# Optimization experiments

Measured on AMD Instinct MI355X. Metric: run time of the kernel, lower is better.

The kernel has to match this reference:

```python
import jax, jax.numpy as jnp
import numpy as np

LAGS = 2
SLOPE = 0.01  # nn.LeakyReLU default negative_slope


def setup_inputs() -> dict:
    key = jax.random.key(0)
    k0, k1, k2, k3, k4 = jax.random.split(key, 5)
    B, T, D, H = 64, 514, 32, 128
    IN = LAGS * D + 1
    x = jax.random.normal(k0, (B, T, D), dtype=jnp.float32)
    # per-latent-dim 2-layer MLP params (num_layers=3, layer_norm=False collapses to 2 Linears)
    W1 = jax.random.normal(k1, (D, H, IN), dtype=jnp.float32) / np.sqrt(IN).astype(np.float32)
    b1 = jax.random.normal(k2, (D, H), dtype=jnp.float32) * 0.01
    W2 = jax.random.normal(k3, (D, H), dtype=jnp.float32) / np.sqrt(H).astype(np.float32)
    b2 = jax.random.normal(k4, (D,), dtype=jnp.float32) * 0.01
    return {"x": x, "W1": W1, "b1": b1, "W2": W2, "b2": b2}


def reference(x, W1, b1, W2, b2):
    L = LAGS
    B, T, D = x.shape
    # unfold(dim=1, size=L+1, step=1) + swapaxes -> windows [B, T-L, L+1, D]
    idx = jnp.arange(T - L)[:, None] + jnp.arange(L + 1)[None, :]
    w = x[:, idx]                       # [B, T-L, L+1, D]
    w = w.reshape(-1, L + 1, D)         # [N, L+1, D]
    yy = w[:, -1, :]                    # [N, D]  current step, per dim
    xx = w[:, :-1, :].reshape(-1, L * D)  # [N, L*D] lagged history (shared)
    # batched tiny-MLP forward: input to g_i is [xx, yy[:, i]]
    pre = (jnp.einsum('nk,dhk->ndh', xx, W1[:, :, :-1])
           + yy[:, :, None] * W1[:, :, -1][None]
           + b1[None])                  # [N, D, H]
    act = jnp.where(pre >= 0, pre, SLOPE * pre)
    residuals = jnp.einsum('ndh,dh->nd', act, W2) + b2[None]  # [N, D]
    # analytic Jacobian of scalar output wrt the (L*D+1)-dim input:
    # J = (W2 * leaky'(pre)) @ W1
    dact = jnp.where(pre >= 0, jnp.float32(1.0), jnp.float32(SLOPE))
    g = dact * W2[None]                 # [N, D, H]
    jac = jnp.einsum('ndh,dhk->ndk', g, W1)  # [N, D, L*D+1]
    logabsdet = jnp.sum(jnp.log(jnp.abs(jac[:, :, -1])), axis=1)  # [N] summed over dims
    # hist_jac: torch returns a list of D tensors [N, 1, L*D]; stacked here as [D, N, 1, L*D]
    hist_jac = jnp.transpose(jac[:, :, :-1], (1, 0, 2))[:, :, None, :]
    residuals = residuals.reshape(B, T - L, D)
    sum_log_abs_det_jacobian = logabsdet.reshape(B, T - L).sum(axis=1)  # [B]
    return residuals, sum_log_abs_det_jacobian, hist_jac
```

## Files before the change

kernel.cpp:

```cpp
#include <hip/hip_runtime.h>
#include <math.h>


typedef _Float16 f16;
typedef __attribute__((ext_vector_type(8))) _Float16 half8;
typedef __attribute__((ext_vector_type(4))) _Float16 half4;
typedef __attribute__((ext_vector_type(4))) float floatx4;

namespace {
constexpr size_t W1F_SZ    = (size_t)32 * 8192 * 2;
constexpr size_t WS_W1F_HI = 0;
constexpr size_t WS_W1F_LO = W1F_SZ;
constexpr size_t WS_W1TF   = 2 * W1F_SZ;
constexpr size_t WS_W64    = 3 * W1F_SZ;
constexpr size_t WS_RES    = WS_W64 + (size_t)32 * 128 * 4;

constexpr int XS_ROW = 40;
constexpr int GB_HP  = 136;

constexpr int L_GB   = 0;
constexpr int L_XSHI = 17408;
constexpr int L_XSLO = L_XSHI + 5280;
constexpr int L_B1   = L_XSLO + 5280;
constexpr int L_W2   = L_B1 + 512;
constexpr int L_W64  = L_W2 + 512;
constexpr int L_YY   = L_W64 + 512;
constexpr int L_RES  = L_YY + 256;
constexpr int L_JAC  = L_RES + 1024;
constexpr int L_TOTAL = L_JAC + 1024;

constexpr size_t OUT1_OFF = (size_t)64 * 512 * 32;
constexpr size_t OUT2_OFF = OUT1_OFF + 64;
}

__global__ __launch_bounds__(256) void split_w1_kernel(
    const float* __restrict__ W1, f16* __restrict__ wh, f16* __restrict__ wl,
    f16* __restrict__ wT, float* __restrict__ w64)
{
    int idx = blockIdx.x * 256 + threadIdx.x;
    if (idx >= 32 * 128 * 64) return;
    int d = idx >> 13, rem = idx & 8191;
    int h = rem >> 6, k = rem & 63;
    float v = W1[((size_t)(d * 128 + h)) * 65 + k];
    f16 hi = (f16)v;
    float r = v - (float)hi;
    int lane1 = (((k >> 3) & 3) << 4) | (h & 15);
    size_t o1 = ((((size_t)d * 8 + (h >> 4)) * 2 + (k >> 5)) * 64 + lane1) * 8 + (k & 7);
    wh[o1] = hi;
    wl[o1] = (f16)(r * 4096.0f);
    int lane2 = (((h >> 3) & 3) << 4) | (k & 15);
    size_t o2 = ((((size_t)d * 4 + (h >> 5)) * 4 + (k >> 4)) * 64 + lane2) * 8 + (h & 7);
    wT[o2] = hi;
    if (k == 63) w64[d * 128 + h] = W1[((size_t)(d * 128 + h)) * 65 + 64];
}

__global__ __launch_bounds__(256, 4) void np_main_kernel(
    const float* __restrict__ x,
    const float* __restrict__ b1,
    const float* __restrict__ W2,
    const float* __restrict__ b2,
    const char* __restrict__ ws,
    float* __restrict__ resw,
    float* __restrict__ out)
{
    extern __shared__ char smem[];
    const int tile = blockIdx.x;
    const int d    = blockIdx.y;
    const int b    = tile >> 3;
    const int t0   = (tile & 7) << 6;
    const int tid  = threadIdx.x;
    const int wave = tid >> 6, lane = tid & 63;
    const int c = lane & 15, q = lane >> 4;

    float* b1L  = (float*)(smem + L_B1);
    float* W2L  = (float*)(smem + L_W2);
    float* w64L = (float*)(smem + L_W64);
    float* yyL  = (float*)(smem + L_YY);
    float* resP = (float*)(smem + L_RES);
    float* jacP = (float*)(smem + L_JAC);

    const f16* w1fh = (const f16*)(ws + WS_W1F_HI) + (size_t)d * 8192;
    const f16* w1fl = (const f16*)(ws + WS_W1F_LO) + (size_t)d * 8192;
    const f16* w1tf = (const f16*)(ws + WS_W1TF)   + (size_t)d * 8192;
    const float* w64p = (const float*)(ws + WS_W64);

    {
        const float4* xs = (const float4*)(x + (size_t)(b * 514 + t0) * 32);
        for (int u = tid; u < 528; u += 256) {
            float4 v = xs[u];
            int row = u >> 3, c4 = u & 7;
            half4 hi, lo;
            #pragma unroll
            for (int j = 0; j < 4; ++j) {
                float vv = (&v.x)[j];
                f16 h = (f16)vv;
                hi[j] = h;
                lo[j] = (f16)((vv - (float)h) * 4096.0f);
            }
            *(half4*)(smem + L_XSHI + (row * XS_ROW + c4 * 4) * 2) = hi;
            *(half4*)(smem + L_XSLO + (row * XS_ROW + c4 * 4) * 2) = lo;
        }
        if (tid < 128) {
            b1L[tid]  = b1[d * 128 + tid];
            W2L[tid]  = W2[d * 128 + tid];
            w64L[tid] = w64p[d * 128 + tid];
        }
        if (tid < 64) yyL[tid] = x[(size_t)(b * 514 + t0 + tid + 2) * 32 + d];
    }
    __syncthreads();

    float yyv[4];
    #pragma unroll
    for (int nt = 0; nt < 4; ++nt) yyv[nt] = yyL[nt * 16 + c];

    float res[4] = {0.f, 0.f, 0.f, 0.f}, j64[4] = {0.f, 0.f, 0.f, 0.f};

    #pragma unroll
    for (int ht = 0; ht < 2; ++ht) {
        floatx4 accP[4], accQ[4];
        #pragma unroll
        for (int nt = 0; nt < 4; ++nt) { accP[nt] = (floatx4)0.f; accQ[nt] = (floatx4)0.f; }

        #pragma unroll
        for (int ks = 0; ks < 2; ++ks) {
            const int fo = (((wave * 2 + ht) * 2 + ks) * 64 + lane) * 8;
            const half8 aH = *(const half8*)(w1fh + fo);
            const half8 aL = *(const half8*)(w1fl + fo);
            half8 bH[4], bL[4];
            #pragma unroll
            for (int nt = 0; nt < 4; ++nt) {
                const int off = (nt * 16 + c + ks) * XS_ROW + q * 8;
                bH[nt] = *(const half8*)(smem + L_XSHI + off * 2);
                bL[nt] = *(const half8*)(smem + L_XSLO + off * 2);
            }
            #pragma unroll
            for (int nt = 0; nt < 4; ++nt) {
                accP[nt] = __builtin_amdgcn_mfma_f32_16x16x32_f16(aH, bH[nt], accP[nt], 0, 0, 0);
                accQ[nt] = __builtin_amdgcn_mfma_f32_16x16x32_f16(aH, bL[nt], accQ[nt], 0, 0, 0);
                accQ[nt] = __builtin_amdgcn_mfma_f32_16x16x32_f16(aL, bH[nt], accQ[nt], 0, 0, 0);
            }
        }

        const int hbase = wave * 32 + ht * 16 + q * 4;
        float b1v[4], W2a[4], W2b[4], w64v[4];
        #pragma unroll
        for (int r = 0; r < 4; ++r) {
            const int h = hbase + r;
            b1v[r]  = b1L[h];
            float w2 = W2L[h];
            W2a[r]  = w2;
            W2b[r]  = 0.01f * w2;
            w64v[r] = w64L[h];
        }

        #pragma unroll
        for (int nt = 0; nt < 4; ++nt) {
            const int n = nt * 16 + c;
            half4 gp;
            #pragma unroll
            for (int r = 0; r < 4; ++r) {
                const float pre = accP[nt][r] + accQ[nt][r] * (1.0f / 4096.0f)
                                + b1v[r] + yyv[nt] * w64v[r];
                const float gg = (pre >= 0.f) ? W2a[r] : W2b[r];
                res[nt] += pre * gg;
                j64[nt] += gg * w64v[r];
                gp[r] = (f16)gg;
            }
            *(half4*)(smem + L_GB + (n * GB_HP + hbase) * 2) = gp;
        }
    }

    #pragma unroll
    for (int nt = 0; nt < 4; ++nt) {
        float rv = res[nt];
        rv += __shfl_xor(rv, 16, 64);
        rv += __shfl_xor(rv, 32, 64);
        float jv = j64[nt];
        jv += __shfl_xor(jv, 16, 64);
        jv += __shfl_xor(jv, 32, 64);
        if (lane < 16) {
            resP[wave * 64 + nt * 16 + lane] = rv;
            jacP[wave * 64 + nt * 16 + lane] = jv;
        }
    }
    __syncthreads();

    if (tid < 64) {
        const int n = tid;
        float r = b2[d], j = 0.f;
        #pragma unroll
        for (int w = 0; w < 4; ++w) { r += resP[w * 64 + n]; j += jacP[w * 64 + n]; }
        resw[(size_t)d * 32768 + (size_t)(b * 512 + t0) + n] = r;
        float lg = logf(fabsf(j));
        #pragma unroll
        for (int off = 32; off > 0; off >>= 1) lg += __shfl_down(lg, off, 64);
        if (tid == 0) atomicAdd(out + OUT1_OFF + b, lg);
    }

    floatx4 acc2[4];
    #pragma unroll
    for (int kt = 0; kt < 4; ++kt) acc2[kt] = (floatx4)0.f;
    #pragma unroll
    for (int ks = 0; ks < 4; ++ks) {
        const half8 aF = *(const half8*)(smem + L_GB + ((wave * 16 + c) * GB_HP + ks * 32 + q * 8) * 2);
        half8 bF[4];
        #pragma unroll
        for (int kt = 0; kt < 4; ++kt)
            bF[kt] = *(const half8*)(w1tf + ((ks * 4 + kt) * 64 + lane) * 8);
        #pragma unroll
        for (int kt = 0; kt < 4; ++kt)
            acc2[kt] = __builtin_amdgcn_mfma_f32_16x16x32_f16(aF, bF[kt], acc2[kt], 0, 0, 0);
    }

    {
        float* tp = (float*)(smem + L_GB + wave * (16 * GB_HP * 2));
        #pragma unroll
        for (int kt = 0; kt < 4; ++kt)
            #pragma unroll
            for (int r = 0; r < 4; ++r)
                tp[(q * 4 + r) * 68 + kt * 16 + c] = acc2[kt][r];
        float* out2 = out + OUT2_OFF + (size_t)d * ((size_t)32768 * 64)
                    + (size_t)(b * 512 + t0 + wave * 16) * 64;
        #pragma unroll
        for (int j = 0; j < 4; ++j) {
            floatx4 v = *(const floatx4*)(tp + (j * 4 + q) * 68 + c * 4);
            *(floatx4*)(out2 + (size_t)j * 256 + (size_t)lane * 4) = v;
        }
    }
}

__global__ __launch_bounds__(256) void finish_res_kernel(
    const float* __restrict__ resw, float* __restrict__ out)
{
    __shared__ float tile[32][65];
    const int n0 = blockIdx.x * 64;
    const int tid = threadIdx.x;
    #pragma unroll
    for (int i = 0; i < 8; ++i) {
        int idx = i * 256 + tid;
        int dd = idx >> 6, n = idx & 63;
        tile[dd][n] = resw[(size_t)dd * 32768 + n0 + n];
    }
    __syncthreads();
    #pragma unroll
    for (int i = 0; i < 8; ++i) {
        int idx = i * 256 + tid;
        int n = idx >> 5, dd = idx & 31;
        out[(size_t)(n0 + n) * 32 + dd] = tile[dd][n];
    }
}

extern "C" void kernel_launch(void* const* d_in, const int* in_sizes, int n_in,
                              void* d_out, int out_size, void* d_ws, size_t ws_size,
                              hipStream_t stream) {
    const float* x  = (const float*)d_in[0];
    const float* W1 = (const float*)d_in[1];
    const float* b1 = (const float*)d_in[2];
    const float* W2 = (const float*)d_in[3];
    const float* b2 = (const float*)d_in[4];
    float* out = (float*)d_out;
    char* ws = (char*)d_ws;

    hipMemsetAsync(out + OUT1_OFF, 0, 64 * sizeof(float), stream);

    hipLaunchKernelGGL(split_w1_kernel, dim3((32 * 128 * 64 + 255) / 256), dim3(256), 0, stream,
                       W1, (f16*)(ws + WS_W1F_HI), (f16*)(ws + WS_W1F_LO),
                       (f16*)(ws + WS_W1TF), (float*)(ws + WS_W64));

    hipLaunchKernelGGL(np_main_kernel, dim3(512, 32), dim3(256), L_TOTAL, stream,
                       x, b1, W2, b2, (const char*)ws, (float*)(ws + WS_RES), out);

    hipLaunchKernelGGL(finish_res_kernel, dim3(512), dim3(256), 0, stream,
                       (const float*)(ws + WS_RES), out);
}
```

Measured before the change: 362.7 us.

## Pack epilogue params into float4 and store Jacobian directly via swapped MFMA operands

The preprocessing kernel now packs b1, W2, 0.01*W2 and the last W1 column into one float4 per hidden unit. The main kernel loads these straight from global memory instead of staging them in LDS. The second MFMA swaps its A/B operands so each lane's accumulator maps to contiguous output columns, which lets the hist_jac tile be written straight from registers without the LDS transpose round-trip. This removes LDS staging and a transpose pass, at the cost of less-coalesced 16-byte stores and extra global loads per wave.

```diff
diff --git a/kernel.cpp b/kernel.cpp
--- a/kernel.cpp
+++ b/kernel.cpp
@@ -12,8 +12,8 @@
 constexpr size_t WS_W1F_HI = 0;
 constexpr size_t WS_W1F_LO = W1F_SZ;
 constexpr size_t WS_W1TF   = 2 * W1F_SZ;
-constexpr size_t WS_W64    = 3 * W1F_SZ;
-constexpr size_t WS_RES    = WS_W64 + (size_t)32 * 128 * 4;
+constexpr size_t WS_EP     = 3 * W1F_SZ;
+constexpr size_t WS_RES    = WS_EP + (size_t)32 * 128 * 16;
 
 constexpr int XS_ROW = 40;
 constexpr int GB_HP  = 136;
@@ -21,10 +21,7 @@
 constexpr int L_GB   = 0;
 constexpr int L_XSHI = 17408;
 constexpr int L_XSLO = L_XSHI + 5280;
-constexpr int L_B1   = L_XSLO + 5280;
-constexpr int L_W2   = L_B1 + 512;
-constexpr int L_W64  = L_W2 + 512;
-constexpr int L_YY   = L_W64 + 512;
+constexpr int L_YY   = L_XSLO + 5280;
 constexpr int L_RES  = L_YY + 256;
 constexpr int L_JAC  = L_RES + 1024;
 constexpr int L_TOTAL = L_JAC + 1024;
@@ -34,8 +31,10 @@
 }
 
 __global__ __launch_bounds__(256) void split_w1_kernel(
-    const float* __restrict__ W1, f16* __restrict__ wh, f16* __restrict__ wl,
-    f16* __restrict__ wT, float* __restrict__ w64)
+    const float* __restrict__ W1, const float* __restrict__ b1,
+    const float* __restrict__ W2,
+    f16* __restrict__ wh, f16* __restrict__ wl,
+    f16* __restrict__ wT, float4* __restrict__ ep)
 {
     int idx = blockIdx.x * 256 + threadIdx.x;
     if (idx >= 32 * 128 * 64) return;
@@ -51,13 +50,20 @@
     int lane2 = (((h >> 3) & 3) << 4) | (k & 15);
     size_t o2 = ((((size_t)d * 4 + (h >> 5)) * 4 + (k >> 4)) * 64 + lane2) * 8 + (h & 7);
     wT[o2] = hi;
-    if (k == 63) w64[d * 128 + h] = W1[((size_t)(d * 128 + h)) * 65 + 64];
+    if (k == 63) {
+        int hh = d * 128 + h;
+        float w2 = W2[hh];
+        float4 e;
+        e.x = b1[hh];
+        e.y = w2;
+        e.z = 0.01f * w2;
+        e.w = W1[(size_t)hh * 65 + 64];
+        ep[hh] = e;
+    }
 }
 
 __global__ __launch_bounds__(256, 4) void np_main_kernel(
     const float* __restrict__ x,
-    const float* __restrict__ b1,
-    const float* __restrict__ W2,
     const float* __restrict__ b2,
     const char* __restrict__ ws,
     float* __restrict__ resw,
@@ -72,9 +78,6 @@
     const int wave = tid >> 6, lane = tid & 63;
     const int c = lane & 15, q = lane >> 4;
 
-    float* b1L  = (float*)(smem + L_B1);
-    float* W2L  = (float*)(smem + L_W2);
-    float* w64L = (float*)(smem + L_W64);
     float* yyL  = (float*)(smem + L_YY);
     float* resP = (float*)(smem + L_RES);
     float* jacP = (float*)(smem + L_JAC);
@@ -82,7 +85,7 @@
     const f16* w1fh = (const f16*)(ws + WS_W1F_HI) + (size_t)d * 8192;
     const f16* w1fl = (const f16*)(ws + WS_W1F_LO) + (size_t)d * 8192;
     const f16* w1tf = (const f16*)(ws + WS_W1TF)   + (size_t)d * 8192;
-    const float* w64p = (const float*)(ws + WS_W64);
+    const float4* epd = (const float4*)(ws + WS_EP) + d * 128;
 
     {
         const float4* xs = (const float4*)(x + (size_t)(b * 514 + t0) * 32);
@@ -100,11 +103,6 @@
             *(half4*)(smem + L_XSHI + (row * XS_ROW + c4 * 4) * 2) = hi;
             *(half4*)(smem + L_XSLO + (row * XS_ROW + c4 * 4) * 2) = lo;
         }
-        if (tid < 128) {
-            b1L[tid]  = b1[d * 128 + tid];
-            W2L[tid]  = W2[d * 128 + tid];
-            w64L[tid] = w64p[d * 128 + tid];
-        }
         if (tid < 64) yyL[tid] = x[(size_t)(b * 514 + t0 + tid + 2) * 32 + d];
     }
     __syncthreads();
@@ -117,6 +115,12 @@
 
     #pragma unroll
     for (int ht = 0; ht < 2; ++ht) {
+        const int hbase = wave * 32 + ht * 16 + q * 4;
+
+        float4 epv[4];
+        #pragma unroll
+        for (int r = 0; r < 4; ++r) epv[r] = epd[hbase + r];
+
         floatx4 accP[4], accQ[4];
         #pragma unroll
         for (int nt = 0; nt < 4; ++nt) { accP[nt] = (floatx4)0.f; accQ[nt] = (floatx4)0.f; }
@@ -141,18 +145,6 @@
             }
         }
 
-        const int hbase = wave * 32 + ht * 16 + q * 4;
-        float b1v[4], W2a[4], W2b[4], w64v[4];
-        #pragma unroll
-        for (int r = 0; r < 4; ++r) {
-            const int h = hbase + r;
-            b1v[r]  = b1L[h];
-            float w2 = W2L[h];
-            W2a[r]  = w2;
-            W2b[r]  = 0.01f * w2;
-            w64v[r] = w64L[h];
-        }
-
         #pragma unroll
         for (int nt = 0; nt < 4; ++nt) {
             const int n = nt * 16 + c;
@@ -160,10 +152,10 @@
             #pragma unroll
             for (int r = 0; r < 4; ++r) {
                 const float pre = accP[nt][r] + accQ[nt][r] * (1.0f / 4096.0f)
-                                + b1v[r] + yyv[nt] * w64v[r];
-                const float gg = (pre >= 0.f) ? W2a[r] : W2b[r];
+                                + epv[r].x + yyv[nt] * epv[r].w;
+                const float gg = (pre >= 0.f) ? epv[r].y : epv[r].z;
                 res[nt] += pre * gg;
-                j64[nt] += gg * w64v[r];
+                j64[nt] += gg * epv[r].w;
                 gp[r] = (f16)gg;
             }
             *(half4*)(smem + L_GB + (n * GB_HP + hbase) * 2) = gp;
@@ -202,30 +194,19 @@
     for (int kt = 0; kt < 4; ++kt) acc2[kt] = (floatx4)0.f;
     #pragma unroll
     for (int ks = 0; ks < 4; ++ks) {
-        const half8 aF = *(const half8*)(smem + L_GB + ((wave * 16 + c) * GB_HP + ks * 32 + q * 8) * 2);
-        half8 bF[4];
-        #pragma unroll
-        for (int kt = 0; kt < 4; ++kt)
-            bF[kt] = *(const half8*)(w1tf + ((ks * 4 + kt) * 64 + lane) * 8);
-        #pragma unroll
-        for (int kt = 0; kt < 4; ++kt)
-            acc2[kt] = __builtin_amdgcn_mfma_f32_16x16x32_f16(aF, bF[kt], acc2[kt], 0, 0, 0);
-    }
-
+        const half8 gF = *(const half8*)(smem + L_GB + ((wave * 16 + c) * GB_HP + ks * 32 + q * 8) * 2);
+        #pragma unroll
+        for (int kt = 0; kt < 4; ++kt) {
+            const half8 wF = *(const half8*)(w1tf + ((ks * 4 + kt) * 64 + lane) * 8);
+            acc2[kt] = __builtin_amdgcn_mfma_f32_16x16x32_f16(wF, gF, acc2[kt], 0, 0, 0);
+        }
+    }
     {
-        float* tp = (float*)(smem + L_GB + wave * (16 * GB_HP * 2));
-        #pragma unroll
-        for (int kt = 0; kt < 4; ++kt)
-            #pragma unroll
-            for (int r = 0; r < 4; ++r)
-                tp[(q * 4 + r) * 68 + kt * 16 + c] = acc2[kt][r];
         float* out2 = out + OUT2_OFF + (size_t)d * ((size_t)32768 * 64)
                     + (size_t)(b * 512 + t0 + wave * 16) * 64;
         #pragma unroll
-        for (int j = 0; j < 4; ++j) {
-            floatx4 v = *(const floatx4*)(tp + (j * 4 + q) * 68 + c * 4);
-            *(floatx4*)(out2 + (size_t)j * 256 + (size_t)lane * 4) = v;
-        }
+        for (int kt = 0; kt < 4; ++kt)
+            *(floatx4*)(out2 + (size_t)c * 64 + kt * 16 + q * 4) = acc2[kt];
     }
 }
 
@@ -264,11 +245,11 @@
     hipMemsetAsync(out + OUT1_OFF, 0, 64 * sizeof(float), stream);
 
     hipLaunchKernelGGL(split_w1_kernel, dim3((32 * 128 * 64 + 255) / 256), dim3(256), 0, stream,
-                       W1, (f16*)(ws + WS_W1F_HI), (f16*)(ws + WS_W1F_LO),
-                       (f16*)(ws + WS_W1TF), (float*)(ws + WS_W64));
+                       W1, b1, W2, (f16*)(ws + WS_W1F_HI), (f16*)(ws + WS_W1F_LO),
+                       (f16*)(ws + WS_W1TF), (float4*)(ws + WS_EP));
 
     hipLaunchKernelGGL(np_main_kernel, dim3(512, 32), dim3(256), L_TOTAL, stream,
-                       x, b1, W2, b2, (const char*)ws, (float*)(ws + WS_RES), out);
+                       x, b2, (const char*)ws, (float*)(ws + WS_RES), out);
 
     hipLaunchKernelGGL(finish_res_kernel, dim3(512), dim3(256), 0, stream,
                        (const float*)(ws + WS_RES), out);
```

New measurement: 372.0 us. +2.6%, slower.
